# Performance work log

Hardware: AMD Instinct MI355X
Metric: run time of the kernel (lower is better)

## Reference

```python
import jax, jax.numpy as jnp
import numpy as np

H = 12            # num_heads
GRID = 14         # sqrt(num_patches)
NP_ = GRID * GRID # num_patches = 196


def _relative_position_index():
    coords = np.stack(np.meshgrid(np.arange(GRID), np.arange(GRID), indexing='ij'))  # [2,14,14]
    flat = coords.reshape(2, -1)                                   # [2,196]
    rel = flat[:, :, None] - flat[:, None, :]                      # [2,196,196]
    rel = rel.transpose(1, 2, 0).astype(np.int32)                  # [196,196,2]
    rel[..., 0] += GRID - 1
    rel[..., 1] += GRID - 1
    rel[..., 0] *= 2 * GRID - 1
    return rel.sum(-1)                                             # [196,196] in [0,729)


def setup_inputs() -> dict:
    key = jax.random.key(0)
    k1, k2, k3, k4 = jax.random.split(key, 4)
    B, N, C = 64, NP_ + 1, 768
    return {
        'x': jax.random.normal(k1, (B, N, C), dtype=jnp.float32),
        'w_qkv': jax.random.normal(k2, (3 * C, C), dtype=jnp.float32) * 0.02,
        'w_proj': jax.random.normal(k3, (C, C), dtype=jnp.float32) * 0.02,
        'b_proj': jnp.zeros((C,), dtype=jnp.float32),
        # torch inits the table to zeros; use small randn so the bias path is exercised
        'rpb_table': jax.random.normal(k4, ((2 * GRID - 1) ** 2, H), dtype=jnp.float32) * 0.02,
        'rel_idx': jnp.asarray(_relative_position_index()),
    }


def reference(x, w_qkv, w_proj, b_proj, rpb_table, rel_idx):
    B, N, C = x.shape
    hd = C // H
    scale = hd ** -0.5
    qkv = (x @ w_qkv.T).reshape(B, N, 3, H, hd).transpose(2, 0, 3, 1, 4)  # [3,B,H,N,hd]
    q, k, v = qkv[0] * scale, qkv[1], qkv[2]
    attn = jnp.einsum('bhqd,bhkd->bhqk', q, k)                            # [B,H,N,N]
    bias = rpb_table[rel_idx.reshape(-1)].reshape(NP_, NP_, H).transpose(2, 0, 1)  # [H,196,196]
    attn = attn.at[:, :, 1:, 1:].add(bias[None])                          # skip CLS row/col
    attn = jax.nn.softmax(attn, axis=-1)
    out = jnp.einsum('bhqk,bhkd->bqhd', attn, v).reshape(B, N, C)
    return out @ w_proj.T + b_proj
```

## Files before the change

kernel.cpp:

```cpp
#include <hip/hip_runtime.h>

typedef float f32x4 __attribute__((ext_vector_type(4)));
typedef short short8 __attribute__((ext_vector_type(8)));

#define DEVI static __device__ __forceinline__

DEVI ushort f2bf(float f) {
  unsigned u = __builtin_bit_cast(unsigned, f);
  u += 0x7fffu + ((u >> 16) & 1u);
  return (ushort)(u >> 16);
}

DEVI short8 pack8(float4 a, float4 b) {
  union { ushort u[8]; short8 v; } t;
  t.u[0] = f2bf(a.x); t.u[1] = f2bf(a.y); t.u[2] = f2bf(a.z); t.u[3] = f2bf(a.w);
  t.u[4] = f2bf(b.x); t.u[5] = f2bf(b.y); t.u[6] = f2bf(b.z); t.u[7] = f2bf(b.w);
  return t.v;
}

DEVI f32x4 MFMA16(short8 a, short8 b, f32x4 c) {
  return __builtin_amdgcn_mfma_f32_16x16x32_bf16(a, b, c, 0, 0, 0);
}

DEVI void gld16(const ushort* g, ushort* l) {
  __builtin_amdgcn_global_load_lds(
      (const __attribute__((address_space(1))) unsigned int*)g,
      (__attribute__((address_space(3))) unsigned int*)l, 16, 0, 0);
}

__global__ void prep_all(const float* __restrict__ table, const int* __restrict__ rel_idx,
                         float* __restrict__ bias,
                         const float* __restrict__ x, ushort* __restrict__ xbf,
                         const float* __restrict__ wq, ushort* __restrict__ wqb,
                         const float* __restrict__ wp, ushort* __restrict__ wpb) {
  const int bid = blockIdx.x, tid = threadIdx.x;
  if (bid < 2028) {
    int i = bid * 256 + tid;
    int k = i % 208;
    int t = i / 208;
    int q = t % 208;
    int h = t / 208;
    float v;
    if (k >= 197) v = -1e30f;
    else if (q == 0 || k == 0 || q >= 197) v = 0.0f;
    else v = table[rel_idx[(q - 1) * 196 + (k - 1)] * 12 + h];
    bias[i] = v;
  } else if (bid < 6756) {
    int i = (bid - 2028) * 256 + tid;
    float4 a = ((const float4*)x)[i * 2];
    float4 b = ((const float4*)x)[i * 2 + 1];
    ((short8*)xbf)[i] = pack8(a, b);
  } else if (bid < 7620) {
    int i = (bid - 6756) * 256 + tid;
    float4 a = ((const float4*)wq)[i * 2];
    float4 b = ((const float4*)wq)[i * 2 + 1];
    ((short8*)wqb)[i] = pack8(a, b);
  } else {
    int i = (bid - 7620) * 256 + tid;
    float4 a = ((const float4*)wp)[i * 2];
    float4 b = ((const float4*)wp)[i * 2 + 1];
    ((short8*)wpb)[i] = pack8(a, b);
  }
}

template <int MODE, int NBN>
__launch_bounds__(256, 3)
__global__ void gemm128(const ushort* __restrict__ A, const ushort* __restrict__ B,
                        ushort* __restrict__ q, ushort* __restrict__ k,
                        ushort* __restrict__ v,
                        const float* __restrict__ bprj, float* __restrict__ out) {
  __shared__ __align__(16) ushort As[3][4096];
  __shared__ __align__(16) ushort Bs[3][4096];

  const int tid = threadIdx.x;
  const int lane = tid & 63, wid = tid >> 6;
  const int wm = wid >> 1, wn = wid & 1;
  const int l15 = lane & 15, l4 = lane >> 4;

  const int nwg = gridDim.x;
  const int qc = nwg >> 3, rc = nwg & 7;
  const int xcd = blockIdx.x & 7, sub = blockIdx.x >> 3;
  const int wgid = (xcd < rc ? xcd * (qc + 1) : rc * (qc + 1) + (xcd - rc) * qc) + sub;
  const int bn = wgid % NBN, bm = wgid / NBN;

  const int c0 = wid * 2, c1 = wid * 2 + 1;
  const int r0 = c0 * 16 + (lane >> 2);
  const int r1 = c1 * 16 + (lane >> 2);
  const int g = lane & 3;
  const int col0 = (g << 3) ^ ((r0 & 6) << 2);
  const int col1 = (g << 3) ^ ((r1 & 6) << 2);
  long ar0 = bm * 128 + r0; if (ar0 > 12607) ar0 = 12607;
  long ar1 = bm * 128 + r1; if (ar1 > 12607) ar1 = 12607;
  const ushort* pA0 = A + ar0 * 768 + col0;
  const ushort* pA1 = A + ar1 * 768 + col1;
  const ushort* pB0 = B + (size_t)(bn * 128 + r0) * 768 + col0;
  const ushort* pB1 = B + (size_t)(bn * 128 + r1) * 768 + col1;

  const int xk = (l4 * 8) ^ ((l15 & 6) << 2);
  int aoff[4], boff[4];
#pragma unroll
  for (int m = 0; m < 4; m++) aoff[m] = (wm * 64 + m * 16 + l15) * 32 + xk;
#pragma unroll
  for (int n = 0; n < 4; n++) boff[n] = (wn * 64 + n * 16 + l15) * 32 + xk;

  f32x4 acc[4][4];
#pragma unroll
  for (int m = 0; m < 4; m++)
#pragma unroll
    for (int n = 0; n < 4; n++) acc[m][n] = (f32x4)0.0f;

#define STAGE(SL, KO)                           \
  gld16(pA0 + (KO), &As[SL][c0 * 512]);         \
  gld16(pA1 + (KO), &As[SL][c1 * 512]);         \
  gld16(pB0 + (KO), &Bs[SL][c0 * 512]);         \
  gld16(pB1 + (KO), &Bs[SL][c1 * 512]);

#define COMPUTE(SL)                                                 \
  {                                                                 \
    short8 af[4], bv[4];                                            \
    _Pragma("unroll") for (int m = 0; m < 4; m++)                   \
        af[m] = *(const short8*)&As[SL][aoff[m]];                   \
    _Pragma("unroll") for (int n = 0; n < 4; n++)                   \
        bv[n] = *(const short8*)&Bs[SL][boff[n]];                   \
    __builtin_amdgcn_s_setprio(1);                                  \
    _Pragma("unroll") for (int m = 0; m < 4; m++)                   \
        _Pragma("unroll") for (int n = 0; n < 4; n++)               \
            acc[m][n] = MFMA16(af[m], bv[n], acc[m][n]);            \
    __builtin_amdgcn_s_setprio(0);                                  \
  }

  STAGE(0, 0)
  STAGE(1, 32)

  int sl_c = 0, sl_s = 2;
  for (int t = 0; t < 22; ++t) {
    asm volatile("s_waitcnt vmcnt(4)" ::: "memory");
    asm volatile("s_waitcnt lgkmcnt(0)" ::: "memory");
    __builtin_amdgcn_s_barrier();
    __builtin_amdgcn_sched_barrier(0);
    STAGE(sl_s, (t + 2) * 32)
    COMPUTE(sl_c)
    sl_c = (sl_c == 2) ? 0 : sl_c + 1;
    sl_s = (sl_s == 2) ? 0 : sl_s + 1;
  }
  asm volatile("s_waitcnt vmcnt(4)" ::: "memory");
  asm volatile("s_waitcnt lgkmcnt(0)" ::: "memory");
  __builtin_amdgcn_s_barrier();
  __builtin_amdgcn_sched_barrier(0);
  COMPUTE(1)
  asm volatile("s_waitcnt vmcnt(0)" ::: "memory");
  asm volatile("s_waitcnt lgkmcnt(0)" ::: "memory");
  __builtin_amdgcn_s_barrier();
  __builtin_amdgcn_sched_barrier(0);
  COMPUTE(2)

  if (MODE == 0) {
    const int s = bn / 6;
    ushort* dst = (s == 0) ? q : ((s == 1) ? k : v);
    const float qs = (s == 0) ? 0.125f : 1.0f;
    const int cbase = bn * 128 + wn * 64 - s * 768;
    const int hh = cbase >> 6;
#pragma unroll
    for (int m = 0; m < 4; m++) {
#pragma unroll
      for (int r = 0; r < 4; r++) {
        int gm = bm * 128 + wm * 64 + m * 16 + l4 * 4 + r;
        if (gm >= 12608) continue;
        int b = gm / 197;
        int ns = gm - b * 197;
        size_t base = (size_t)((b * 12 + hh) * 197 + ns) * 64;
#pragma unroll
        for (int n = 0; n < 4; n++)
          dst[base + n * 16 + l15] = f2bf(acc[m][n][r] * qs);
      }
    }
  } else {
    float bb[4];
#pragma unroll
    for (int n = 0; n < 4; n++) bb[n] = bprj[bn * 128 + wn * 64 + n * 16 + l15];
#pragma unroll
    for (int m = 0; m < 4; m++) {
#pragma unroll
      for (int r = 0; r < 4; r++) {
        int gm = bm * 128 + wm * 64 + m * 16 + l4 * 4 + r;
        if (gm >= 12608) continue;
#pragma unroll
        for (int n = 0; n < 4; n++)
          out[(size_t)gm * 768 + bn * 128 + wn * 64 + n * 16 + l15] = acc[m][n][r] + bb[n];
      }
    }
  }
#undef STAGE
#undef COMPUTE
}

__launch_bounds__(512)
__global__ void attn(const ushort* __restrict__ qws, const ushort* __restrict__ kws,
                     const ushort* __restrict__ vws, const float* __restrict__ biasws,
                     ushort* __restrict__ aout) {
  __shared__ __align__(16) ushort Ks[208 * 72];
  __shared__ __align__(16) ushort Vt[64 * 232];
  __shared__ __align__(16) ushort Ps[8 * 16 * 232];

  const int bh = blockIdx.x;
  const int b = bh / 12;
  const int h = bh - b * 12;
  const ushort* qb = qws + (size_t)bh * 197 * 64;
  const ushort* kb = kws + (size_t)bh * 197 * 64;
  const ushort* vb = vws + (size_t)bh * 197 * 64;

  const int tid = threadIdx.x;
  const int lane = tid & 63, wid = tid >> 6;
  const int l15 = lane & 15, l4 = lane >> 4;

  for (int c = tid; c < 208 * 8; c += 512) {
    int n = c >> 3, col = (c & 7) << 3;
    short8 v = (short8)0;
    if (n < 197) v = *(const short8*)(kb + n * 64 + col);
    *(short8*)&Ks[n * 72 + col] = v;
  }
  for (int c = tid; c < 224 * 8; c += 512) {
    int n = c % 224;
    int d0 = (c / 224) << 3;
    ushort tmp[8] = {0, 0, 0, 0, 0, 0, 0, 0};
    if (n < 197) {
      short8 v = *(const short8*)(vb + n * 64 + d0);
#pragma unroll
      for (int j = 0; j < 8; j++) tmp[j] = (ushort)v[j];
    }
#pragma unroll
    for (int j = 0; j < 8; j++) Vt[(d0 + j) * 232 + n] = tmp[j];
  }
  __syncthreads();

  ushort* pb = &Ps[wid * (16 * 232)];
  const float* biasb = biasws + (size_t)h * 208 * 208;

  for (int t = wid; t < 13; t += 8) {
    const int q0 = t * 16;
    int qr = q0 + l15; if (qr > 196) qr = 196;
    short8 aq0 = *(const short8*)(qb + qr * 64 + (l4 << 3));
    short8 aq1 = *(const short8*)(qb + qr * 64 + 32 + (l4 << 3));

    f32x4 sc[13];
    __builtin_amdgcn_s_setprio(1);
#pragma unroll
    for (int ct = 0; ct < 13; ct++) {
      short8 b0 = *(const short8*)&Ks[(ct * 16 + l15) * 72 + (l4 << 3)];
      short8 b1 = *(const short8*)&Ks[(ct * 16 + l15) * 72 + 32 + (l4 << 3)];
      f32x4 s = (f32x4)0.0f;
      s = MFMA16(aq0, b0, s);
      s = MFMA16(aq1, b1, s);
      sc[ct] = s;
    }
    __builtin_amdgcn_s_setprio(0);

    float mx[4] = {-1e38f, -1e38f, -1e38f, -1e38f};
#pragma unroll
    for (int ct = 0; ct < 13; ct++) {
#pragma unroll
      for (int r = 0; r < 4; r++) {
        float bv = biasb[(q0 + l4 * 4 + r) * 208 + ct * 16 + l15];
        float v = sc[ct][r] + bv;
        sc[ct][r] = v;
        mx[r] = fmaxf(mx[r], v);
      }
    }
#pragma unroll
    for (int r = 0; r < 4; r++) {
      mx[r] = fmaxf(mx[r], __shfl_xor(mx[r], 1));
      mx[r] = fmaxf(mx[r], __shfl_xor(mx[r], 2));
      mx[r] = fmaxf(mx[r], __shfl_xor(mx[r], 4));
      mx[r] = fmaxf(mx[r], __shfl_xor(mx[r], 8));
    }
    float sum[4] = {0.f, 0.f, 0.f, 0.f};
#pragma unroll
    for (int ct = 0; ct < 13; ct++) {
#pragma unroll
      for (int r = 0; r < 4; r++) {
        float p = __expf(sc[ct][r] - mx[r]);
        sc[ct][r] = p;
        sum[r] += p;
      }
    }
#pragma unroll
    for (int r = 0; r < 4; r++) {
      sum[r] += __shfl_xor(sum[r], 1);
      sum[r] += __shfl_xor(sum[r], 2);
      sum[r] += __shfl_xor(sum[r], 4);
      sum[r] += __shfl_xor(sum[r], 8);
    }

#pragma unroll
    for (int ct = 0; ct < 13; ct++)
#pragma unroll
      for (int r = 0; r < 4; r++)
        pb[(l4 * 4 + r) * 232 + ct * 16 + l15] = f2bf(sc[ct][r]);
#pragma unroll
    for (int r = 0; r < 4; r++)
      pb[(l4 * 4 + r) * 232 + 208 + l15] = 0;

    short8 pa[7];
#pragma unroll
    for (int kk = 0; kk < 7; kk++)
      pa[kk] = *(const short8*)&pb[l15 * 232 + kk * 32 + (l4 << 3)];
    f32x4 o[4];
    __builtin_amdgcn_s_setprio(1);
#pragma unroll
    for (int dt = 0; dt < 4; dt++) {
      f32x4 acc = (f32x4)0.0f;
#pragma unroll
      for (int kk = 0; kk < 7; kk++) {
        short8 bv = *(const short8*)&Vt[(dt * 16 + l15) * 232 + kk * 32 + (l4 << 3)];
        acc = MFMA16(pa[kk], bv, acc);
      }
      o[dt] = acc;
    }
    __builtin_amdgcn_s_setprio(0);

    float rs[4];
#pragma unroll
    for (int r = 0; r < 4; r++) rs[r] = 1.0f / sum[r];
#pragma unroll
    for (int dt = 0; dt < 4; dt++) {
#pragma unroll
      for (int r = 0; r < 4; r++) {
        int row = q0 + l4 * 4 + r;
        if (row < 197) {
          float v = o[dt][r] * rs[r];
          aout[(size_t)(b * 197 + row) * 768 + h * 64 + dt * 16 + l15] = f2bf(v);
        }
      }
    }
  }
}

extern "C" void kernel_launch(void* const* d_in, const int* in_sizes, int n_in,
                              void* d_out, int out_size, void* d_ws, size_t ws_size,
                              hipStream_t stream) {
  const float* x      = (const float*)d_in[0];
  const float* w_qkv  = (const float*)d_in[1];
  const float* w_proj = (const float*)d_in[2];
  const float* b_proj = (const float*)d_in[3];
  const float* rpb    = (const float*)d_in[4];
  const int*   relidx = (const int*)d_in[5];
  float* out = (float*)d_out;

  char* ws = (char*)d_ws;
  const size_t HB = (size_t)12608 * 768 * 2;
  ushort* xbf   = (ushort*)(ws);
  ushort* qws   = (ushort*)(ws + HB);
  ushort* kws   = (ushort*)(ws + 2 * HB);
  ushort* vws   = (ushort*)(ws + 3 * HB);
  float*  bias  = (float*)(ws + 4 * HB);
  ushort* wqkvb = (ushort*)(ws + 4 * HB + 2076672);
  ushort* wprjb = (ushort*)(ws + 4 * HB + 2076672 + 3538944);
  ushort* aout  = xbf;

  hipLaunchKernelGGL(prep_all, dim3(7908), dim3(256), 0, stream,
                     rpb, relidx, bias, x, xbf, w_qkv, wqkvb, w_proj, wprjb);
  hipLaunchKernelGGL((gemm128<0, 18>), dim3(18 * 99), dim3(256), 0, stream,
                     xbf, wqkvb, qws, kws, vws, nullptr, nullptr);
  hipLaunchKernelGGL(attn, dim3(768), dim3(512), 0, stream, qws, kws, vws, bias, aout);
  hipLaunchKernelGGL((gemm128<1, 6>), dim3(6 * 99), dim3(256), 0, stream,
                     aout, wprjb, nullptr, nullptr, nullptr, b_proj, out);
}
```

Before: 145.1 us.

## Store bias in bf16, double-buffer GEMM, use 13 waves in attention

```diff
diff --git a/kernel.cpp b/kernel.cpp
--- a/kernel.cpp
+++ b/kernel.cpp
@@ -9,6 +9,11 @@
   unsigned u = __builtin_bit_cast(unsigned, f);
   u += 0x7fffu + ((u >> 16) & 1u);
   return (ushort)(u >> 16);
+}
+
+DEVI float b2f(ushort u) {
+  unsigned x = ((unsigned)u) << 16;
+  return __builtin_bit_cast(float, x);
 }
 
 DEVI short8 pack8(float4 a, float4 b) {
@@ -28,8 +33,11 @@
       (__attribute__((address_space(3))) unsigned int*)l, 16, 0, 0);
 }
 
+#define VMC0() asm volatile("s_waitcnt vmcnt(0)" ::: "memory")
+#define LGK0() asm volatile("s_waitcnt lgkmcnt(0)" ::: "memory")
+
 __global__ void prep_all(const float* __restrict__ table, const int* __restrict__ rel_idx,
-                         float* __restrict__ bias,
+                         ushort* __restrict__ bias,
                          const float* __restrict__ x, ushort* __restrict__ xbf,
                          const float* __restrict__ wq, ushort* __restrict__ wqb,
                          const float* __restrict__ wp, ushort* __restrict__ wpb) {
@@ -44,7 +52,7 @@
     if (k >= 197) v = -1e30f;
     else if (q == 0 || k == 0 || q >= 197) v = 0.0f;
     else v = table[rel_idx[(q - 1) * 196 + (k - 1)] * 12 + h];
-    bias[i] = v;
+    bias[i] = f2bf(v);
   } else if (bid < 6756) {
     int i = (bid - 2028) * 256 + tid;
     float4 a = ((const float4*)x)[i * 2];
@@ -64,13 +72,13 @@
 }
 
 template <int MODE, int NBN>
-__launch_bounds__(256, 3)
+__launch_bounds__(256, 4)
 __global__ void gemm128(const ushort* __restrict__ A, const ushort* __restrict__ B,
                         ushort* __restrict__ q, ushort* __restrict__ k,
                         ushort* __restrict__ v,
                         const float* __restrict__ bprj, float* __restrict__ out) {
-  __shared__ __align__(16) ushort As[3][4096];
-  __shared__ __align__(16) ushort Bs[3][4096];
+  __shared__ __align__(16) ushort As[2][4096];
+  __shared__ __align__(16) ushort Bs[2][4096];
 
   const int tid = threadIdx.x;
   const int lane = tid & 63, wid = tid >> 6;
@@ -109,19 +117,19 @@
 #pragma unroll
     for (int n = 0; n < 4; n++) acc[m][n] = (f32x4)0.0f;
 
-#define STAGE(SL, KO)                           \
-  gld16(pA0 + (KO), &As[SL][c0 * 512]);         \
-  gld16(pA1 + (KO), &As[SL][c1 * 512]);         \
-  gld16(pB0 + (KO), &Bs[SL][c0 * 512]);         \
-  gld16(pB1 + (KO), &Bs[SL][c1 * 512]);
-
-#define COMPUTE(SL)                                                 \
+#define STAGE(BUF, KO)                          \
+  gld16(pA0 + (KO), &As[BUF][c0 * 512]);        \
+  gld16(pA1 + (KO), &As[BUF][c1 * 512]);        \
+  gld16(pB0 + (KO), &Bs[BUF][c0 * 512]);        \
+  gld16(pB1 + (KO), &Bs[BUF][c1 * 512]);
+
+#define COMPUTE(BUF)                                                \
   {                                                                 \
     short8 af[4], bv[4];                                            \
     _Pragma("unroll") for (int m = 0; m < 4; m++)                   \
-        af[m] = *(const short8*)&As[SL][aoff[m]];                   \
+        af[m] = *(const short8*)&As[BUF][aoff[m]];                  \
     _Pragma("unroll") for (int n = 0; n < 4; n++)                   \
-        bv[n] = *(const short8*)&Bs[SL][boff[n]];                   \
+        bv[n] = *(const short8*)&Bs[BUF][boff[n]];                  \
     __builtin_amdgcn_s_setprio(1);                                  \
     _Pragma("unroll") for (int m = 0; m < 4; m++)                   \
         _Pragma("unroll") for (int n = 0; n < 4; n++)               \
@@ -130,29 +138,17 @@
   }
 
   STAGE(0, 0)
-  STAGE(1, 32)
-
-  int sl_c = 0, sl_s = 2;
-  for (int t = 0; t < 22; ++t) {
-    asm volatile("s_waitcnt vmcnt(4)" ::: "memory");
-    asm volatile("s_waitcnt lgkmcnt(0)" ::: "memory");
+  for (int t = 0; t < 23; ++t) {
+    VMC0(); LGK0();
     __builtin_amdgcn_s_barrier();
     __builtin_amdgcn_sched_barrier(0);
-    STAGE(sl_s, (t + 2) * 32)
-    COMPUTE(sl_c)
-    sl_c = (sl_c == 2) ? 0 : sl_c + 1;
-    sl_s = (sl_s == 2) ? 0 : sl_s + 1;
-  }
-  asm volatile("s_waitcnt vmcnt(4)" ::: "memory");
-  asm volatile("s_waitcnt lgkmcnt(0)" ::: "memory");
+    STAGE((t + 1) & 1, (t + 1) * 32)
+    COMPUTE(t & 1)
+  }
+  VMC0(); LGK0();
   __builtin_amdgcn_s_barrier();
   __builtin_amdgcn_sched_barrier(0);
   COMPUTE(1)
-  asm volatile("s_waitcnt vmcnt(0)" ::: "memory");
-  asm volatile("s_waitcnt lgkmcnt(0)" ::: "memory");
-  __builtin_amdgcn_s_barrier();
-  __builtin_amdgcn_sched_barrier(0);
-  COMPUTE(2)
 
   if (MODE == 0) {
     const int s = bn / 6;
@@ -194,13 +190,13 @@
 #undef COMPUTE
 }
 
-__launch_bounds__(512)
+__launch_bounds__(832)
 __global__ void attn(const ushort* __restrict__ qws, const ushort* __restrict__ kws,
-                     const ushort* __restrict__ vws, const float* __restrict__ biasws,
+                     const ushort* __restrict__ vws, const ushort* __restrict__ biasws,
                      ushort* __restrict__ aout) {
   __shared__ __align__(16) ushort Ks[208 * 72];
   __shared__ __align__(16) ushort Vt[64 * 232];
-  __shared__ __align__(16) ushort Ps[8 * 16 * 232];
+  __shared__ __align__(16) ushort Ps[13 * 16 * 232];
 
   const int bh = blockIdx.x;
   const int b = bh / 12;
@@ -213,13 +209,13 @@
   const int lane = tid & 63, wid = tid >> 6;
   const int l15 = lane & 15, l4 = lane >> 4;
 
-  for (int c = tid; c < 208 * 8; c += 512) {
+  for (int c = tid; c < 208 * 8; c += 832) {
     int n = c >> 3, col = (c & 7) << 3;
     short8 v = (short8)0;
     if (n < 197) v = *(const short8*)(kb + n * 64 + col);
     *(short8*)&Ks[n * 72 + col] = v;
   }
-  for (int c = tid; c < 224 * 8; c += 512) {
+  for (int c = tid; c < 224 * 8; c += 832) {
     int n = c % 224;
     int d0 = (c / 224) << 3;
     ushort tmp[8] = {0, 0, 0, 0, 0, 0, 0, 0};
@@ -234,9 +230,10 @@
   __syncthreads();
 
   ushort* pb = &Ps[wid * (16 * 232)];
-  const float* biasb = biasws + (size_t)h * 208 * 208;
-
-  for (int t = wid; t < 13; t += 8) {
+  const ushort* biasb = biasws + (size_t)h * 208 * 208;
+
+  {
+    const int t = wid;
     const int q0 = t * 16;
     int qr = q0 + l15; if (qr > 196) qr = 196;
     short8 aq0 = *(const short8*)(qb + qr * 64 + (l4 << 3));
@@ -260,7 +257,7 @@
     for (int ct = 0; ct < 13; ct++) {
 #pragma unroll
       for (int r = 0; r < 4; r++) {
-        float bv = biasb[(q0 + l4 * 4 + r) * 208 + ct * 16 + l15];
+        float bv = b2f(biasb[(q0 + l4 * 4 + r) * 208 + ct * 16 + l15]);
         float v = sc[ct][r] + bv;
         sc[ct][r] = v;
         mx[r] = fmaxf(mx[r], v);
@@ -352,7 +349,7 @@
   ushort* qws   = (ushort*)(ws + HB);
   ushort* kws   = (ushort*)(ws + 2 * HB);
   ushort* vws   = (ushort*)(ws + 3 * HB);
-  float*  bias  = (float*)(ws + 4 * HB);
+  ushort* bias  = (ushort*)(ws + 4 * HB);
   ushort* wqkvb = (ushort*)(ws + 4 * HB + 2076672);
   ushort* wprjb = (ushort*)(ws + 4 * HB + 2076672 + 3538944);
   ushort* aout  = xbf;
@@ -361,7 +358,7 @@
                      rpb, relidx, bias, x, xbf, w_qkv, wqkvb, w_proj, wprjb);
   hipLaunchKernelGGL((gemm128<0, 18>), dim3(18 * 99), dim3(256), 0, stream,
                      xbf, wqkvb, qws, kws, vws, nullptr, nullptr);
-  hipLaunchKernelGGL(attn, dim3(768), dim3(512), 0, stream, qws, kws, vws, bias, aout);
+  hipLaunchKernelGGL(attn, dim3(768), dim3(832), 0, stream, qws, kws, vws, bias, aout);
   hipLaunchKernelGGL((gemm128<1, 6>), dim3(6 * 99), dim3(256), 0, stream,
                      aout, wprjb, nullptr, nullptr, nullptr, b_proj, out);
 }
```

Measured after the change: 132.5 us, median of 4. 1.09x faster.
